# Performance work log

Measured on AMD Instinct MI355X. Metric: run time of the kernel, lower is better.

## Reference

```python
import jax, jax.numpy as jnp
import numpy as np

NFEAT, NHID = 128, 128

def setup_inputs() -> dict:
    key = jax.random.key(0)
    k1, k2, k3, k4 = jax.random.split(key, 4)
    x = jax.random.normal(k1, (32, 1024, NFEAT), dtype=jnp.float32)
    adj = jax.random.uniform(k2, (32, 1024, 1024), dtype=jnp.float32)
    # GraphConvolution parameters (Kipf init ~ uniform, scale irrelevant for correctness)
    bound = 1.0 / np.sqrt(NHID)
    W = jax.random.uniform(k3, (NFEAT, NHID), dtype=jnp.float32, minval=-bound, maxval=bound)
    b = jax.random.uniform(k4, (NHID,), dtype=jnp.float32, minval=-bound, maxval=bound)
    return {"x": x, "adj": adj, "W": W, "b": b}

def reference(x, adj, W, b):
    # Batched equivalent of the per-sample python loop:
    # out[i] = relu(adj[i] @ (x[i] @ W) + b); dropout is identity in eval mode.
    support = jnp.einsum('bnf,fh->bnh', x, W)          # [B, N, nhid]
    out = jnp.einsum('bnm,bmh->bnh', adj, support) + b  # [B, N, nhid]
    return jax.nn.relu(out)
```

## Files before the change

### kernel.cpp

```cpp
#include <hip/hip_runtime.h>
#include <stdint.h>


typedef short bf16x8 __attribute__((ext_vector_type(8)));
typedef float f32x4 __attribute__((ext_vector_type(4)));
typedef unsigned short u16x8 __attribute__((ext_vector_type(8)));

__device__ __forceinline__ unsigned short f2bf(float f) {
    uint32_t u = __builtin_bit_cast(uint32_t, f);
    u += 0x7FFFu + ((u >> 16) & 1u);
    return (unsigned short)(u >> 16);
}

__device__ __forceinline__ bf16x8 cvt8(f32x4 v0, f32x4 v1) {
    u16x8 p;
    p[0] = f2bf(v0.x); p[1] = f2bf(v0.y); p[2] = f2bf(v0.z); p[3] = f2bf(v0.w);
    p[4] = f2bf(v1.x); p[5] = f2bf(v1.y); p[6] = f2bf(v1.z); p[7] = f2bf(v1.w);
    return __builtin_bit_cast(bf16x8, p);
}

__global__ __launch_bounds__(256) void k0_wt(const float* __restrict__ W,
                                             unsigned short* __restrict__ WT) {
    int o = blockIdx.x * 256 + threadIdx.x;
    int h = o >> 7, f = o & 127;
    WT[o] = f2bf(W[f * 128 + h]);
}

__global__ __launch_bounds__(256) void k1_support(const float* __restrict__ x,
                                                  const unsigned short* __restrict__ WT,
                                                  unsigned short* __restrict__ ST) {
    int t = threadIdx.x;
    int wv = t >> 6, lane = t & 63, l16 = lane & 15, quad = lane >> 4;
    int wave_h = (wv & 1) * 64, wave_m = (wv >> 1) * 32;
    int node_base = blockIdx.x * 64;
    const float* xb = x + (size_t)node_base * 128;

    f32x4 acc[4][2];
#pragma unroll
    for (int ht = 0; ht < 4; ++ht)
#pragma unroll
        for (int mt = 0; mt < 2; ++mt) acc[ht][mt] = 0.f;

#pragma unroll
    for (int s = 0; s < 4; ++s) {
        int ko = s * 32 + quad * 8;
        bf16x8 a[4], bb[2];
#pragma unroll
        for (int ht = 0; ht < 4; ++ht)
            a[ht] = *(const bf16x8*)&WT[(wave_h + ht * 16 + l16) * 128 + ko];
#pragma unroll
        for (int mt = 0; mt < 2; ++mt) {
            const float* xr = xb + (size_t)(wave_m + mt * 16 + l16) * 128 + ko;
            bb[mt] = cvt8(*(const f32x4*)xr, *(const f32x4*)(xr + 4));
        }
#pragma unroll
        for (int ht = 0; ht < 4; ++ht)
#pragma unroll
            for (int mt = 0; mt < 2; ++mt)
                acc[ht][mt] = __builtin_amdgcn_mfma_f32_16x16x32_bf16(
                    a[ht], bb[mt], acc[ht][mt], 0, 0, 0);
    }

    int batch = blockIdx.x >> 4;
    int m_in_b = (blockIdx.x & 15) * 64;
#pragma unroll
    for (int ht = 0; ht < 4; ++ht)
#pragma unroll
        for (int mt = 0; mt < 2; ++mt) {
            int mcol = wave_m + mt * 16 + l16;
#pragma unroll
            for (int r = 0; r < 4; ++r) {
                int h = wave_h + ht * 16 + quad * 4 + r;
                ST[(((size_t)batch * 128 + h) << 10) + m_in_b + mcol] =
                    f2bf(acc[ht][mt][r]);
            }
        }
}

__global__ __launch_bounds__(256) void k2_gcn(const float* __restrict__ adj,
                                              const unsigned short* __restrict__ ST,
                                              const float* __restrict__ bias,
                                              float* __restrict__ out) {
    int t = threadIdx.x;
    int batch = blockIdx.x >> 4;
    int mbase = (blockIdx.x & 15) * 64;
    int wv = t >> 6, lane = t & 63, l16 = lane & 15, quad = lane >> 4;
    int wave_m = (wv & 1) * 32, wave_n = (wv >> 1) * 64;

    float bv[4];
#pragma unroll
    for (int j = 0; j < 4; ++j) bv[j] = bias[wave_n + j * 16 + l16];

    f32x4 acc[2][4];
#pragma unroll
    for (int i = 0; i < 2; ++i)
#pragma unroll
        for (int j = 0; j < 4; ++j) acc[i][j] = 0.f;

    const float* adjb = adj + ((size_t)batch * 1024 + mbase) * 1024;
    const unsigned short* stb = ST + ((size_t)batch * 128) * 1024;

    for (int kb = 0; kb < 16; ++kb) {
#pragma unroll
        for (int s = 0; s < 2; ++s) {
            int ko = kb * 64 + s * 32 + quad * 8;
            bf16x8 a[2], bb[4];
#pragma unroll
            for (int i = 0; i < 2; ++i) {
                const float* ar = adjb + (size_t)(wave_m + i * 16 + l16) * 1024 + ko;
                a[i] = cvt8(*(const f32x4*)ar, *(const f32x4*)(ar + 4));
            }
#pragma unroll
            for (int j = 0; j < 4; ++j)
                bb[j] = *(const bf16x8*)&stb[(size_t)(wave_n + j * 16 + l16) * 1024 + ko];
#pragma unroll
            for (int i = 0; i < 2; ++i)
#pragma unroll
                for (int j = 0; j < 4; ++j)
                    acc[i][j] = __builtin_amdgcn_mfma_f32_16x16x32_bf16(
                        a[i], bb[j], acc[i][j], 0, 0, 0);
        }
    }

    float* outb = out + ((size_t)batch * 1024 + mbase) * 128;
#pragma unroll
    for (int i = 0; i < 2; ++i)
#pragma unroll
        for (int j = 0; j < 4; ++j) {
            int n = wave_n + j * 16 + l16;
#pragma unroll
            for (int r = 0; r < 4; ++r) {
                int m = wave_m + i * 16 + quad * 4 + r;
                float v = acc[i][j][r] + bv[j];
                outb[(size_t)m * 128 + n] = fmaxf(v, 0.f);
            }
        }
}

extern "C" void kernel_launch(void* const* d_in, const int* in_sizes, int n_in,
                              void* d_out, int out_size, void* d_ws, size_t ws_size,
                              hipStream_t stream) {
    const float* x = (const float*)d_in[0];
    const float* adj = (const float*)d_in[1];
    const float* W = (const float*)d_in[2];
    const float* b = (const float*)d_in[3];
    float* out = (float*)d_out;

    unsigned short* ST = (unsigned short*)d_ws;
    unsigned short* WT = (unsigned short*)d_ws + (size_t)32 * 128 * 1024;

    k0_wt<<<64, 256, 0, stream>>>(W, WT);
    k1_support<<<512, 256, 0, stream>>>(x, WT, ST);
    k2_gcn<<<512, 256, 0, stream>>>(adj, ST, b, out);
}
```

Baseline: 247.5 us.

## Stage adj and support tiles through LDS in GCN aggregation kernel

The aggregation kernel now loads each 64-wide K chunk of adj (converted to bf16) and the support tile cooperatively into padded shared memory, then feeds MFMAs from LDS. This replaces per-wave direct global loads, which were strided and partly duplicated. The block tile shrinks from 64 to 32 rows and the grid doubles to 1024 blocks, so the support matrix is re-read more times. The K loop also gains two barriers per step with no double buffering, so loads are not overlapped with compute.

```diff
diff --git a/kernel.cpp b/kernel.cpp
--- a/kernel.cpp
+++ b/kernel.cpp
@@ -4,6 +4,8 @@
 
 typedef short bf16x8 __attribute__((ext_vector_type(8)));
 typedef float f32x4 __attribute__((ext_vector_type(4)));
+typedef int i32x4 __attribute__((ext_vector_type(4)));
+typedef unsigned short u16x4 __attribute__((ext_vector_type(4)));
 typedef unsigned short u16x8 __attribute__((ext_vector_type(8)));
 
 __device__ __forceinline__ unsigned short f2bf(float f) {
@@ -77,60 +79,79 @@
         }
 }
 
+#define K2S 72
 __global__ __launch_bounds__(256) void k2_gcn(const float* __restrict__ adj,
                                               const unsigned short* __restrict__ ST,
                                               const float* __restrict__ bias,
                                               float* __restrict__ out) {
+    __shared__ __align__(16) unsigned short As[32 * K2S];
+    __shared__ __align__(16) unsigned short Bs[128 * K2S];
     int t = threadIdx.x;
-    int batch = blockIdx.x >> 4;
-    int mbase = (blockIdx.x & 15) * 64;
+    int batch = blockIdx.x >> 5;
+    int mbase = (blockIdx.x & 31) * 32;
     int wv = t >> 6, lane = t & 63, l16 = lane & 15, quad = lane >> 4;
-    int wave_m = (wv & 1) * 32, wave_n = (wv >> 1) * 64;
+    int wave_n = wv * 32;
 
-    float bv[4];
+    float bv[2];
 #pragma unroll
-    for (int j = 0; j < 4; ++j) bv[j] = bias[wave_n + j * 16 + l16];
+    for (int j = 0; j < 2; ++j) bv[j] = bias[wave_n + j * 16 + l16];
 
-    f32x4 acc[2][4];
+    f32x4 acc[2][2];
 #pragma unroll
     for (int i = 0; i < 2; ++i)
 #pragma unroll
-        for (int j = 0; j < 4; ++j) acc[i][j] = 0.f;
+        for (int j = 0; j < 2; ++j) acc[i][j] = 0.f;
 
     const float* adjb = adj + ((size_t)batch * 1024 + mbase) * 1024;
     const unsigned short* stb = ST + ((size_t)batch * 128) * 1024;
 
     for (int kb = 0; kb < 16; ++kb) {
 #pragma unroll
+        for (int i = 0; i < 2; ++i) {
+            int c = i * 256 + t;
+            int row = c >> 4, c4 = c & 15;
+            f32x4 v = *(const f32x4*)(adjb + (size_t)row * 1024 + kb * 64 + c4 * 4);
+            u16x4 p;
+            p.x = f2bf(v.x); p.y = f2bf(v.y); p.z = f2bf(v.z); p.w = f2bf(v.w);
+            *(u16x4*)&As[row * K2S + c4 * 4] = p;
+        }
+#pragma unroll
+        for (int i = 0; i < 4; ++i) {
+            int c = i * 256 + t;
+            int row = c >> 3, ch = c & 7;
+            *(i32x4*)&Bs[row * K2S + ch * 8] =
+                *(const i32x4*)(stb + (size_t)row * 1024 + kb * 64 + ch * 8);
+        }
+        __syncthreads();
+#pragma unroll
         for (int s = 0; s < 2; ++s) {
-            int ko = kb * 64 + s * 32 + quad * 8;
-            bf16x8 a[2], bb[4];
+            int ko = s * 32 + quad * 8;
+            bf16x8 a[2], bb[2];
 #pragma unroll
-            for (int i = 0; i < 2; ++i) {
-                const float* ar = adjb + (size_t)(wave_m + i * 16 + l16) * 1024 + ko;
-                a[i] = cvt8(*(const f32x4*)ar, *(const f32x4*)(ar + 4));
-            }
+            for (int i = 0; i < 2; ++i)
+                a[i] = *(const bf16x8*)&As[(i * 16 + l16) * K2S + ko];
 #pragma unroll
-            for (int j = 0; j < 4; ++j)
-                bb[j] = *(const bf16x8*)&stb[(size_t)(wave_n + j * 16 + l16) * 1024 + ko];
+            for (int j = 0; j < 2; ++j)
+                bb[j] = *(const bf16x8*)&Bs[(wave_n + j * 16 + l16) * K2S + ko];
 #pragma unroll
             for (int i = 0; i < 2; ++i)
 #pragma unroll
-                for (int j = 0; j < 4; ++j)
+                for (int j = 0; j < 2; ++j)
                     acc[i][j] = __builtin_amdgcn_mfma_f32_16x16x32_bf16(
                         a[i], bb[j], acc[i][j], 0, 0, 0);
         }
+        __syncthreads();
     }
 
     float* outb = out + ((size_t)batch * 1024 + mbase) * 128;
 #pragma unroll
     for (int i = 0; i < 2; ++i)
 #pragma unroll
-        for (int j = 0; j < 4; ++j) {
+        for (int j = 0; j < 2; ++j) {
             int n = wave_n + j * 16 + l16;
 #pragma unroll
             for (int r = 0; r < 4; ++r) {
-                int m = wave_m + i * 16 + quad * 4 + r;
+                int m = i * 16 + quad * 4 + r;
                 float v = acc[i][j][r] + bv[j];
                 outb[(size_t)m * 128 + n] = fmaxf(v, 0.f);
             }
@@ -151,5 +172,5 @@
 
     k0_wt<<<64, 256, 0, stream>>>(W, WT);
     k1_support<<<512, 256, 0, stream>>>(x, WT, ST);
-    k2_gcn<<<512, 256, 0, stream>>>(adj, ST, b, out);
+    k2_gcn<<<1024, 256, 0, stream>>>(adj, ST, b, out);
 }
```

Measured after the change: 230.0 us. -7.1%, faster.

## Stage adj and support tiles through double-buffered LDS in GCN kernel

Applied to the files above, without the earlier changes.

The aggregation kernel now loads adj and support tiles with coalesced row-wise global reads. It converts adj to bf16 once and writes both tiles into padded, double-buffered shared memory. MFMA operands are then read from LDS, and global loads for the next k-blocks are issued before the current block's MFMAs so memory latency overlaps with compute. This removes duplicated, strided global reads across waves, at the cost of about 55KB of LDS per block, extra barriers, and a launch bound that targets two blocks per CU.

```diff
diff --git a/kernel.cpp b/kernel.cpp
--- a/kernel.cpp
+++ b/kernel.cpp
@@ -4,6 +4,8 @@
 
 typedef short bf16x8 __attribute__((ext_vector_type(8)));
 typedef float f32x4 __attribute__((ext_vector_type(4)));
+typedef int i32x4 __attribute__((ext_vector_type(4)));
+typedef unsigned short u16x4 __attribute__((ext_vector_type(4)));
 typedef unsigned short u16x8 __attribute__((ext_vector_type(8)));
 
 __device__ __forceinline__ unsigned short f2bf(float f) {
@@ -18,6 +20,13 @@
     p[4] = f2bf(v1.x); p[5] = f2bf(v1.y); p[6] = f2bf(v1.z); p[7] = f2bf(v1.w);
     return __builtin_bit_cast(bf16x8, p);
 }
+
+#define BAR_LGKM()                                                \
+    do {                                                          \
+        asm volatile("s_waitcnt lgkmcnt(0)" ::: "memory");        \
+        __builtin_amdgcn_s_barrier();                             \
+        asm volatile("" ::: "memory");                            \
+    } while (0)
 
 __global__ __launch_bounds__(256) void k0_wt(const float* __restrict__ W,
                                              unsigned short* __restrict__ WT) {
@@ -77,10 +86,13 @@
         }
 }
 
-__global__ __launch_bounds__(256) void k2_gcn(const float* __restrict__ adj,
-                                              const unsigned short* __restrict__ ST,
-                                              const float* __restrict__ bias,
-                                              float* __restrict__ out) {
+#define K2S 72
+__global__ __launch_bounds__(256, 2) void k2_gcn(const float* __restrict__ adj,
+                                                 const unsigned short* __restrict__ ST,
+                                                 const float* __restrict__ bias,
+                                                 float* __restrict__ out) {
+    __shared__ __align__(16) unsigned short As[2][64 * K2S];
+    __shared__ __align__(16) unsigned short Bs[2][128 * K2S];
     int t = threadIdx.x;
     int batch = blockIdx.x >> 4;
     int mbase = (blockIdx.x & 15) * 64;
@@ -100,25 +112,70 @@
     const float* adjb = adj + ((size_t)batch * 1024 + mbase) * 1024;
     const unsigned short* stb = ST + ((size_t)batch * 128) * 1024;
 
-    for (int kb = 0; kb < 16; ++kb) {
+    int ar_row = t >> 4, ar_c4 = t & 15;
+    int sr_row = t >> 3, sr_ch = t & 7;
+
+    f32x4 avA[4], avB[4];
+    i32x4 svA[4], svB[4];
+
+    auto LOAD = [&](int kb, f32x4 (&av)[4], i32x4 (&sv)[4]) {
+#pragma unroll
+        for (int i = 0; i < 4; ++i)
+            av[i] = *(const f32x4*)(adjb + (size_t)(i * 16 + ar_row) * 1024 +
+                                    kb * 64 + ar_c4 * 4);
+#pragma unroll
+        for (int i = 0; i < 4; ++i)
+            sv[i] = *(const i32x4*)(stb + (size_t)(i * 32 + sr_row) * 1024 +
+                                    kb * 64 + sr_ch * 8);
+    };
+    auto WRITE = [&](int buf, f32x4 (&av)[4], i32x4 (&sv)[4]) {
+#pragma unroll
+        for (int i = 0; i < 4; ++i) {
+            u16x4 p;
+            p.x = f2bf(av[i].x); p.y = f2bf(av[i].y);
+            p.z = f2bf(av[i].z); p.w = f2bf(av[i].w);
+            *(u16x4*)&As[buf][(i * 16 + ar_row) * K2S + ar_c4 * 4] = p;
+        }
+#pragma unroll
+        for (int i = 0; i < 4; ++i)
+            *(i32x4*)&Bs[buf][(i * 32 + sr_row) * K2S + sr_ch * 8] = sv[i];
+    };
+    auto MFMA = [&](int buf) {
 #pragma unroll
         for (int s = 0; s < 2; ++s) {
-            int ko = kb * 64 + s * 32 + quad * 8;
+            int ko = s * 32 + quad * 8;
             bf16x8 a[2], bb[4];
 #pragma unroll
-            for (int i = 0; i < 2; ++i) {
-                const float* ar = adjb + (size_t)(wave_m + i * 16 + l16) * 1024 + ko;
-                a[i] = cvt8(*(const f32x4*)ar, *(const f32x4*)(ar + 4));
-            }
+            for (int i = 0; i < 2; ++i)
+                a[i] = *(const bf16x8*)&As[buf][(wave_m + i * 16 + l16) * K2S + ko];
 #pragma unroll
             for (int j = 0; j < 4; ++j)
-                bb[j] = *(const bf16x8*)&stb[(size_t)(wave_n + j * 16 + l16) * 1024 + ko];
+                bb[j] = *(const bf16x8*)&Bs[buf][(wave_n + j * 16 + l16) * K2S + ko];
 #pragma unroll
             for (int i = 0; i < 2; ++i)
 #pragma unroll
                 for (int j = 0; j < 4; ++j)
                     acc[i][j] = __builtin_amdgcn_mfma_f32_16x16x32_bf16(
                         a[i], bb[j], acc[i][j], 0, 0, 0);
+        }
+    };
+
+    LOAD(0, avA, svA);
+    WRITE(0, avA, svA);
+    LOAD(1, avB, svB);
+    BAR_LGKM();
+
+    for (int j = 0; j < 8; ++j) {
+        int kb = 2 * j;
+        if (kb + 2 < 16) LOAD(kb + 2, avA, svA);
+        MFMA(0);
+        WRITE(1, avB, svB);
+        BAR_LGKM();
+        if (kb + 3 < 16) LOAD(kb + 3, avB, svB);
+        MFMA(1);
+        if (kb + 1 < 15) {
+            WRITE(0, avA, svA);
+            BAR_LGKM();
         }
     }
 
```

Measured after the change: 228.2 us. -7.8%, faster.

## Restructure GCN aggregation waves to own 16 rows with adj register prefetch

Applied to the files above, without the earlier changes.

Each wave now computes 16 output rows across all 128 hidden columns, instead of a 32x64 tile. Each adj element is therefore loaded by exactly one wave, while every wave reads the full support matrix. The next k-block of adj is prefetched into registers while the current one is converted and fed to MFMA, and the loop is fully unrolled with launch_bounds(256,2). This targets latency on the dominant fp32 adj stream. In exchange it doubles ST reads per wave and adds register pressure from 16 bf16x8 B fragments plus the prefetch buffers.

```diff
diff --git a/kernel.cpp b/kernel.cpp
--- a/kernel.cpp
+++ b/kernel.cpp
@@ -77,64 +77,75 @@
         }
 }
 
-__global__ __launch_bounds__(256) void k2_gcn(const float* __restrict__ adj,
-                                              const unsigned short* __restrict__ ST,
-                                              const float* __restrict__ bias,
-                                              float* __restrict__ out) {
+__global__ __launch_bounds__(256, 2) void k2_gcn(const float* __restrict__ adj,
+                                                 const unsigned short* __restrict__ ST,
+                                                 const float* __restrict__ bias,
+                                                 float* __restrict__ out) {
     int t = threadIdx.x;
     int batch = blockIdx.x >> 4;
     int mbase = (blockIdx.x & 15) * 64;
     int wv = t >> 6, lane = t & 63, l16 = lane & 15, quad = lane >> 4;
-    int wave_m = (wv & 1) * 32, wave_n = (wv >> 1) * 64;
+    int wrow = mbase + wv * 16;
 
-    float bv[4];
-#pragma unroll
-    for (int j = 0; j < 4; ++j) bv[j] = bias[wave_n + j * 16 + l16];
-
-    f32x4 acc[2][4];
-#pragma unroll
-    for (int i = 0; i < 2; ++i)
-#pragma unroll
-        for (int j = 0; j < 4; ++j) acc[i][j] = 0.f;
-
-    const float* adjb = adj + ((size_t)batch * 1024 + mbase) * 1024;
+    const float* adjw = adj + ((size_t)batch * 1024 + wrow + l16) * 1024;
     const unsigned short* stb = ST + ((size_t)batch * 128) * 1024;
 
+    float bv[8];
+#pragma unroll
+    for (int j = 0; j < 8; ++j) bv[j] = bias[j * 16 + l16];
+
+    f32x4 acc[8];
+#pragma unroll
+    for (int j = 0; j < 8; ++j) acc[j] = 0.f;
+
+    f32x4 aC[4], aN[4];
+
+#pragma unroll
+    for (int s = 0; s < 2; ++s) {
+        const float* p = adjw + s * 32 + quad * 8;
+        aC[s * 2] = *(const f32x4*)p;
+        aC[s * 2 + 1] = *(const f32x4*)(p + 4);
+    }
+
+#pragma unroll
     for (int kb = 0; kb < 16; ++kb) {
+        bf16x8 bb[8][2];
 #pragma unroll
-        for (int s = 0; s < 2; ++s) {
-            int ko = kb * 64 + s * 32 + quad * 8;
-            bf16x8 a[2], bb[4];
+        for (int j = 0; j < 8; ++j)
 #pragma unroll
-            for (int i = 0; i < 2; ++i) {
-                const float* ar = adjb + (size_t)(wave_m + i * 16 + l16) * 1024 + ko;
-                a[i] = cvt8(*(const f32x4*)ar, *(const f32x4*)(ar + 4));
+            for (int s = 0; s < 2; ++s)
+                bb[j][s] = *(const bf16x8*)&stb[(size_t)(j * 16 + l16) * 1024 +
+                                                kb * 64 + s * 32 + quad * 8];
+        if (kb < 15) {
+#pragma unroll
+            for (int s = 0; s < 2; ++s) {
+                const float* p = adjw + (kb + 1) * 64 + s * 32 + quad * 8;
+                aN[s * 2] = *(const f32x4*)p;
+                aN[s * 2 + 1] = *(const f32x4*)(p + 4);
             }
+        }
+        bf16x8 a0 = cvt8(aC[0], aC[1]);
+        bf16x8 a1 = cvt8(aC[2], aC[3]);
 #pragma unroll
-            for (int j = 0; j < 4; ++j)
-                bb[j] = *(const bf16x8*)&stb[(size_t)(wave_n + j * 16 + l16) * 1024 + ko];
+        for (int j = 0; j < 8; ++j) {
+            acc[j] = __builtin_amdgcn_mfma_f32_16x16x32_bf16(a0, bb[j][0], acc[j], 0, 0, 0);
+            acc[j] = __builtin_amdgcn_mfma_f32_16x16x32_bf16(a1, bb[j][1], acc[j], 0, 0, 0);
+        }
 #pragma unroll
-            for (int i = 0; i < 2; ++i)
-#pragma unroll
-                for (int j = 0; j < 4; ++j)
-                    acc[i][j] = __builtin_amdgcn_mfma_f32_16x16x32_bf16(
-                        a[i], bb[j], acc[i][j], 0, 0, 0);
-        }
+        for (int i = 0; i < 4; ++i) aC[i] = aN[i];
     }
 
     float* outb = out + ((size_t)batch * 1024 + mbase) * 128;
 #pragma unroll
-    for (int i = 0; i < 2; ++i)
+    for (int j = 0; j < 8; ++j) {
+        int n = j * 16 + l16;
 #pragma unroll
-        for (int j = 0; j < 4; ++j) {
-            int n = wave_n + j * 16 + l16;
-#pragma unroll
-            for (int r = 0; r < 4; ++r) {
-                int m = wave_m + i * 16 + quad * 4 + r;
-                float v = acc[i][j][r] + bv[j];
-                outb[(size_t)m * 128 + n] = fmaxf(v, 0.f);
-            }
+        for (int r = 0; r < 4; ++r) {
+            int m = wv * 16 + quad * 4 + r;
+            float v = acc[j][r] + bv[j];
+            outb[(size_t)m * 128 + n] = fmaxf(v, 0.f);
         }
+    }
 }
 
 extern "C" void kernel_launch(void* const* d_in, const int* in_sizes, int n_in,
```

Result: slower. 263.3 us (+6.4%).
